# Kernel optimization log

Measured on AMD Instinct MI355X. Metric: run time of the kernel, lower is better.

Reference implementation:

```python
import jax, jax.numpy as jnp
import numpy as np


def _gcn_layer(x, W, b, row, col, num_nodes):
    # x: [N, F_in]; W: [F_in, F_out]; row/col: [E2] (with self-loops appended)
    xw = x @ W  # [N, F_out]
    ones = jnp.ones(row.shape[0], dtype=xw.dtype)
    deg = jax.ops.segment_sum(ones, col, num_segments=num_nodes)  # in-degree incl. self-loop
    dinv = jnp.where(deg > 0, jax.lax.rsqrt(deg), 0.0)
    norm = dinv[row] * dinv[col]  # [E2]
    msg = xw[row] * norm[:, None]  # gather + per-edge scale
    out = jax.ops.segment_sum(msg, col, num_segments=num_nodes)  # scatter-add to targets
    return out + b


def setup_inputs() -> dict:
    key = jax.random.key(0)
    k1, k2, k3, k4, k5 = jax.random.split(key, 5)
    N, E, F_in, F_hid = 100000, 640000, 128, 128
    x = jax.random.normal(k1, (N, F_in), dtype=jnp.float32)
    edge_index = jax.random.randint(k2, (2, E), 0, N, dtype=jnp.int64)
    # Glorot-style init like PyG GCNConv
    s1 = (6.0 / (F_in + F_hid)) ** 0.5
    W1 = jax.random.uniform(k3, (F_in, F_hid), jnp.float32, -s1, s1)
    b1 = jnp.zeros((F_hid,), jnp.float32)
    s2 = (6.0 / (F_hid + F_hid)) ** 0.5
    W2 = jax.random.uniform(k4, (F_hid, F_hid), jnp.float32, -s2, s2)
    b2 = jnp.zeros((F_hid,), jnp.float32)
    return {"x": x, "edge_index": edge_index, "W1": W1, "b1": b1, "W2": W2, "b2": b2}


def reference(x, edge_index, W1, b1, W2, b2):
    N = x.shape[0]
    # GCN adds self-loops before symmetric normalization (add_self_loops=True default)
    self_idx = jnp.arange(N, dtype=edge_index.dtype)
    row = jnp.concatenate([edge_index[0], self_idx])
    col = jnp.concatenate([edge_index[1], self_idx])
    h = _gcn_layer(x, W1, b1, row, col, N)
    h = jax.nn.relu(h)
    # dropout is identity in eval mode (training=False)
    out = _gcn_layer(h, W2, b2, row, col, N)
    return out
```

## Files before the change

### kernel.cpp

```cpp
#include <hip/hip_runtime.h>
#include <cstdint>
#include <cstddef>


typedef unsigned int u32;
typedef unsigned short u16;
typedef __attribute__((ext_vector_type(8))) short short8;
typedef __attribute__((ext_vector_type(4))) float f32x4;

__device__ __forceinline__ float bf2f(u32 lo16) {
  union { u32 u; float f; } c; c.u = lo16 << 16; return c.f;
}
__device__ __forceinline__ u32 f2bf(float f) {
  union { float f; u32 u; } c; c.f = f;
  return (c.u + 0x7fffu + ((c.u >> 16) & 1u)) >> 16;
}

__global__ __launch_bounds__(256) void zero_i32_kernel(int* __restrict__ p, int n) {
  int i = blockIdx.x * 256 + threadIdx.x;
  if (i < n) p[i] = 0;
}

__global__ __launch_bounds__(256) void count_kernel(
    const int* __restrict__ cols, const int* __restrict__ rows,
    int* __restrict__ cnt, int E, int N) {
  int e = blockIdx.x * 256 + threadIdx.x;
  if (e >= E) return;
  int c = cols[e];
  int r = rows[e];
  if ((unsigned)c >= (unsigned)N || (unsigned)r >= (unsigned)N) return;
  atomicAdd(&cnt[c], 1);
}

__global__ __launch_bounds__(256) void dinv_kernel(
    const int* __restrict__ cnt, float* __restrict__ dinv, int N) {
  int i = blockIdx.x * 256 + threadIdx.x;
  if (i >= N) return;
  dinv[i] = rsqrtf((float)cnt[i] + 1.0f);
}

__global__ __launch_bounds__(256) void wt_kernel(
    const float* __restrict__ W, u16* __restrict__ Wt) {
  int idx = blockIdx.x * 256 + threadIdx.x;
  int k = idx >> 7, n = idx & 127;
  Wt[n * 128 + k] = (u16)f2bf(W[idx]);
}

__global__ __launch_bounds__(256) void scan1_kernel(
    const int* __restrict__ cnt, int* __restrict__ rowptr,
    int* __restrict__ bsum, int N) {
  __shared__ int sd[256];
  int t = threadIdx.x;
  int base = blockIdx.x * 1024 + t * 4;
  int c0 = (base + 0 < N) ? cnt[base + 0] : 0;
  int c1 = (base + 1 < N) ? cnt[base + 1] : 0;
  int c2 = (base + 2 < N) ? cnt[base + 2] : 0;
  int c3 = (base + 3 < N) ? cnt[base + 3] : 0;
  int s = c0 + c1 + c2 + c3;
  sd[t] = s;
  __syncthreads();
  for (int off = 1; off < 256; off <<= 1) {
    int v = (t >= off) ? sd[t - off] : 0;
    __syncthreads();
    sd[t] += v;
    __syncthreads();
  }
  int excl = sd[t] - s;
  if (base + 0 < N) rowptr[base + 0] = excl;
  if (base + 1 < N) rowptr[base + 1] = excl + c0;
  if (base + 2 < N) rowptr[base + 2] = excl + c0 + c1;
  if (base + 3 < N) rowptr[base + 3] = excl + c0 + c1 + c2;
  if (t == 255) bsum[blockIdx.x] = sd[255];
}

__global__ __launch_bounds__(128) void scan2_kernel(
    const int* __restrict__ bsum, int* __restrict__ bsum2,
    int* __restrict__ rowptr, int NB, int N) {
  __shared__ int sd[128];
  int t = threadIdx.x;
  int v = (t < NB) ? bsum[t] : 0;
  sd[t] = v;
  __syncthreads();
  for (int off = 1; off < 128; off <<= 1) {
    int u = (t >= off) ? sd[t - off] : 0;
    __syncthreads();
    sd[t] += u;
    __syncthreads();
  }
  bsum2[t] = sd[t] - v;
  if (t == NB - 1) rowptr[N] = sd[t];
}

__global__ __launch_bounds__(256) void scan3_kernel(
    int* __restrict__ rowptr, const int* __restrict__ bsum2, int N) {
  int t = threadIdx.x;
  int b = blockIdx.x;
  int base = b * 1024 + t * 4;
  int add = bsum2[b];
#pragma unroll
  for (int k = 0; k < 4; k++)
    if (base + k < N) rowptr[base + k] += add;
}

__global__ __launch_bounds__(256) void fill_kernel(
    const int* __restrict__ cols, const int* __restrict__ rows,
    const int* __restrict__ rowptr, int* __restrict__ cursor,
    int* __restrict__ adj, int E, int N) {
  int e = blockIdx.x * 256 + threadIdx.x;
  if (e >= E) return;
  int c = cols[e];
  int r = rows[e];
  if ((unsigned)c >= (unsigned)N || (unsigned)r >= (unsigned)N) return;
  int pos = atomicAdd(&cursor[c], 1);
  adj[rowptr[c] + pos] = r;
}

template <int A_BF16>
__global__ __launch_bounds__(256) void gemm_mfma_kernel(
    const void* __restrict__ Av, const u16* __restrict__ Wt,
    const float* __restrict__ dinv, u16* __restrict__ C, int M) {
  __shared__ u16 Ws[128][136];
  __shared__ float dv_s[128];
  const int tid = threadIdx.x;
  const int row0 = blockIdx.x * 128;

  {
    const uint4* src = (const uint4*)Wt;
#pragma unroll
    for (int i = 0; i < 8; i++) {
      int linear = tid + i * 256;
      int n = linear >> 4;
      int kq = linear & 15;
      *(uint4*)&Ws[n][kq * 8] = src[linear];
    }
  }
  if (tid < 128) {
    int gr = row0 + tid;
    dv_s[tid] = (gr < M) ? dinv[gr] : 0.f;
  }
  __syncthreads();

  const int wave = tid >> 6;
  const int lane = tid & 63;
  const int lm = lane & 15;
  const int quad = lane >> 4;
  const int m0 = wave * 32;

  f32x4 acc[2][8];
#pragma unroll
  for (int mt = 0; mt < 2; mt++)
#pragma unroll
    for (int nt = 0; nt < 8; nt++) acc[mt][nt] = (f32x4){0.f, 0.f, 0.f, 0.f};

#pragma unroll
  for (int k0 = 0; k0 < 128; k0 += 32) {
    short8 bfrag[8];
#pragma unroll
    for (int nt = 0; nt < 8; nt++)
      bfrag[nt] = *(const short8*)&Ws[nt * 16 + lm][k0 + quad * 8];

    short8 afrag[2];
#pragma unroll
    for (int mt = 0; mt < 2; mt++) {
      int gr = row0 + m0 + mt * 16 + lm;
      short8 f = (short8){0, 0, 0, 0, 0, 0, 0, 0};
      if (gr < M) {
        if (A_BF16) {
          f = *(const short8*)((const u16*)Av + (size_t)gr * 128 + k0 + quad * 8);
        } else {
          const float* Af = (const float*)Av + (size_t)gr * 128 + k0 + quad * 8;
          float4 v0 = *(const float4*)Af;
          float4 v1 = *(const float4*)(Af + 4);
          f[0] = (short)f2bf(v0.x); f[1] = (short)f2bf(v0.y);
          f[2] = (short)f2bf(v0.z); f[3] = (short)f2bf(v0.w);
          f[4] = (short)f2bf(v1.x); f[5] = (short)f2bf(v1.y);
          f[6] = (short)f2bf(v1.z); f[7] = (short)f2bf(v1.w);
        }
      }
      afrag[mt] = f;
    }

#pragma unroll
    for (int mt = 0; mt < 2; mt++)
#pragma unroll
      for (int nt = 0; nt < 8; nt++)
        acc[mt][nt] = __builtin_amdgcn_mfma_f32_16x16x32_bf16(
            afrag[mt], bfrag[nt], acc[mt][nt], 0, 0, 0);
  }

#pragma unroll
  for (int mt = 0; mt < 2; mt++) {
    int rbase = m0 + mt * 16 + quad * 4;
#pragma unroll
    for (int r = 0; r < 4; r++) {
      int lrow = rbase + r;
      int grow = row0 + lrow;
      if (grow < M) {
        float dv = dv_s[lrow];
        u16* Crow = C + (size_t)grow * 128 + lm;
#pragma unroll
        for (int nt = 0; nt < 8; nt++)
          Crow[nt * 16] = (u16)f2bf(acc[mt][nt][r] * dv);
      }
    }
  }
}

template <int RELU, int OUT_BF16>
__global__ __launch_bounds__(256) void aggregate_kernel(
    const u32* __restrict__ xws, const int* __restrict__ rowptr,
    const int* __restrict__ adj, const float* __restrict__ dinv,
    const float* __restrict__ bias, void* __restrict__ out, int N) {
  int node = blockIdx.x * 4 + (threadIdx.x >> 6);
  if (node >= N) return;
  int lane = threadIdx.x & 63;

  u32 sv = xws[(size_t)node * 64 + lane];
  float accx = bf2f(sv & 0xffff);
  float accy = bf2f(sv >> 16);

  int beg = rowptr[node];
  int end = rowptr[node + 1];
  int j = beg;
  for (; j + 4 <= end; j += 4) {
    int s0 = adj[j], s1 = adj[j + 1], s2 = adj[j + 2], s3 = adj[j + 3];
    float m0 = 1.f, m1 = 1.f, m2 = 1.f, m3 = 1.f;
    if ((unsigned)s0 >= (unsigned)N) { s0 = 0; m0 = 0.f; }
    if ((unsigned)s1 >= (unsigned)N) { s1 = 0; m1 = 0.f; }
    if ((unsigned)s2 >= (unsigned)N) { s2 = 0; m2 = 0.f; }
    if ((unsigned)s3 >= (unsigned)N) { s3 = 0; m3 = 0.f; }
    u32 v0 = xws[(size_t)s0 * 64 + lane];
    u32 v1 = xws[(size_t)s1 * 64 + lane];
    u32 v2 = xws[(size_t)s2 * 64 + lane];
    u32 v3 = xws[(size_t)s3 * 64 + lane];
    accx = fmaf(m0, bf2f(v0 & 0xffff), accx); accy = fmaf(m0, bf2f(v0 >> 16), accy);
    accx = fmaf(m1, bf2f(v1 & 0xffff), accx); accy = fmaf(m1, bf2f(v1 >> 16), accy);
    accx = fmaf(m2, bf2f(v2 & 0xffff), accx); accy = fmaf(m2, bf2f(v2 >> 16), accy);
    accx = fmaf(m3, bf2f(v3 & 0xffff), accx); accy = fmaf(m3, bf2f(v3 >> 16), accy);
  }
  for (; j < end; j++) {
    int s = adj[j];
    float m = 1.f;
    if ((unsigned)s >= (unsigned)N) { s = 0; m = 0.f; }
    u32 v = xws[(size_t)s * 64 + lane];
    accx = fmaf(m, bf2f(v & 0xffff), accx);
    accy = fmaf(m, bf2f(v >> 16), accy);
  }

  float di = dinv[node];
  float2 bv = ((const float2*)bias)[lane];
  float ox = fmaf(di, accx, bv.x);
  float oy = fmaf(di, accy, bv.y);
  if (RELU) { ox = fmaxf(ox, 0.f); oy = fmaxf(oy, 0.f); }
  if (OUT_BF16) {
    ((u32*)out)[(size_t)node * 64 + lane] = f2bf(ox) | (f2bf(oy) << 16);
  } else {
    ((float2*)out)[(size_t)node * 64 + lane] = make_float2(ox, oy);
  }
}

extern "C" void kernel_launch(void* const* d_in, const int* in_sizes, int n_in,
                              void* d_out, int out_size, void* d_ws, size_t ws_size,
                              hipStream_t stream) {
  const float* x  = (const float*)d_in[0];
  const int*   ei = (const int*)d_in[1];
  const float* W1 = (const float*)d_in[2];
  const float* b1 = (const float*)d_in[3];
  const float* W2 = (const float*)d_in[4];
  const float* b2 = (const float*)d_in[5];
  float* out = (float*)d_out;

  const int F = 128;
  const int N = in_sizes[0] / F;
  const int E = in_sizes[1] / 2;
  const int* rows = ei;
  const int* cols = ei + E;

  u16*   bufXW  = (u16*)d_ws;
  u16*   bufH   = bufXW + (size_t)N * F;
  float* dinv   = (float*)(bufH + (size_t)N * F);
  int*   cnt    = (int*)(dinv + N);
  int*   rowptr = cnt + N;
  int*   adj    = rowptr + (N + 1);
  int*   bsum   = adj + E;
  int*   bsum2  = bsum + 128;
  u16*   Wt1    = (u16*)(bsum2 + 128);
  u16*   Wt2    = Wt1 + 128 * 128;

  const int NB = (N + 1023) / 1024;
  int eblocks = (E + 255) / 256;
  int nblocks = (N + 255) / 256;

  zero_i32_kernel<<<nblocks, 256, 0, stream>>>(cnt, N);
  count_kernel<<<eblocks, 256, 0, stream>>>(cols, rows, cnt, E, N);
  dinv_kernel<<<nblocks, 256, 0, stream>>>(cnt, dinv, N);
  scan1_kernel<<<NB, 256, 0, stream>>>(cnt, rowptr, bsum, N);
  scan2_kernel<<<1, 128, 0, stream>>>(bsum, bsum2, rowptr, NB, N);
  scan3_kernel<<<NB, 256, 0, stream>>>(rowptr, bsum2, N);
  zero_i32_kernel<<<nblocks, 256, 0, stream>>>(cnt, N);
  fill_kernel<<<eblocks, 256, 0, stream>>>(cols, rows, rowptr, cnt, adj, E, N);
  wt_kernel<<<64, 256, 0, stream>>>(W1, Wt1);
  wt_kernel<<<64, 256, 0, stream>>>(W2, Wt2);

  int gblocks = (N + 127) / 128;
  int ablocks = (N + 3) / 4;
  gemm_mfma_kernel<0><<<gblocks, 256, 0, stream>>>(x, Wt1, dinv, bufXW, N);
  aggregate_kernel<1, 1><<<ablocks, 256, 0, stream>>>(
      (const u32*)bufXW, rowptr, adj, dinv, b1, bufH, N);
  gemm_mfma_kernel<1><<<gblocks, 256, 0, stream>>>(bufH, Wt2, dinv, bufXW, N);
  aggregate_kernel<0, 0><<<ablocks, 256, 0, stream>>>(
      (const u32*)bufXW, rowptr, adj, dinv, b2, out, N);
}
```

Baseline: 292.5 us.

## Fuse setup kernels, stage GEMM output via LDS, widen aggregate gather per lane

Folds the dinv computation into scan1, merges the two weight-transpose launches into one, and reuses the count array as a decrementing cursor in fill so the second zeroing pass goes away. The GEMM epilogue now stages bf16 results in shared memory and writes them as coalesced 16-byte stores instead of scattered 2-byte stores. The aggregation kernel uses 32 lanes per node, each loading 8 bytes, and gathers 8 neighbours per iteration to raise memory-level parallelism. In exchange the edge order within each adjacency list is reversed, which can change floating-point summation order.

```diff
diff --git a/kernel.cpp b/kernel.cpp
--- a/kernel.cpp
+++ b/kernel.cpp
@@ -32,23 +32,20 @@
   atomicAdd(&cnt[c], 1);
 }
 
-__global__ __launch_bounds__(256) void dinv_kernel(
-    const int* __restrict__ cnt, float* __restrict__ dinv, int N) {
-  int i = blockIdx.x * 256 + threadIdx.x;
-  if (i >= N) return;
-  dinv[i] = rsqrtf((float)cnt[i] + 1.0f);
-}
-
 __global__ __launch_bounds__(256) void wt_kernel(
-    const float* __restrict__ W, u16* __restrict__ Wt) {
-  int idx = blockIdx.x * 256 + threadIdx.x;
+    const float* __restrict__ W1, const float* __restrict__ W2,
+    u16* __restrict__ Wt1, u16* __restrict__ Wt2) {
+  int b = blockIdx.x;
+  const float* W = (b < 64) ? W1 : W2;
+  u16* Wt = (b < 64) ? Wt1 : Wt2;
+  int idx = (b & 63) * 256 + threadIdx.x;
   int k = idx >> 7, n = idx & 127;
   Wt[n * 128 + k] = (u16)f2bf(W[idx]);
 }
 
 __global__ __launch_bounds__(256) void scan1_kernel(
     const int* __restrict__ cnt, int* __restrict__ rowptr,
-    int* __restrict__ bsum, int N) {
+    int* __restrict__ bsum, float* __restrict__ dinv, int N) {
   __shared__ int sd[256];
   int t = threadIdx.x;
   int base = blockIdx.x * 1024 + t * 4;
@@ -56,6 +53,10 @@
   int c1 = (base + 1 < N) ? cnt[base + 1] : 0;
   int c2 = (base + 2 < N) ? cnt[base + 2] : 0;
   int c3 = (base + 3 < N) ? cnt[base + 3] : 0;
+  if (base + 0 < N) dinv[base + 0] = rsqrtf((float)c0 + 1.0f);
+  if (base + 1 < N) dinv[base + 1] = rsqrtf((float)c1 + 1.0f);
+  if (base + 2 < N) dinv[base + 2] = rsqrtf((float)c2 + 1.0f);
+  if (base + 3 < N) dinv[base + 3] = rsqrtf((float)c3 + 1.0f);
   int s = c0 + c1 + c2 + c3;
   sd[t] = s;
   __syncthreads();
@@ -104,15 +105,15 @@
 
 __global__ __launch_bounds__(256) void fill_kernel(
     const int* __restrict__ cols, const int* __restrict__ rows,
-    const int* __restrict__ rowptr, int* __restrict__ cursor,
+    const int* __restrict__ rowptr, int* __restrict__ cnt,
     int* __restrict__ adj, int E, int N) {
   int e = blockIdx.x * 256 + threadIdx.x;
   if (e >= E) return;
   int c = cols[e];
   int r = rows[e];
   if ((unsigned)c >= (unsigned)N || (unsigned)r >= (unsigned)N) return;
-  int pos = atomicAdd(&cursor[c], 1);
-  adj[rowptr[c] + pos] = r;
+  int pos = atomicSub(&cnt[c], 1) - 1;
+  if (pos >= 0) adj[rowptr[c] + pos] = r;
 }
 
 template <int A_BF16>
@@ -188,74 +189,87 @@
             afrag[mt], bfrag[nt], acc[mt][nt], 0, 0, 0);
   }
 
+  __syncthreads();
 #pragma unroll
   for (int mt = 0; mt < 2; mt++) {
     int rbase = m0 + mt * 16 + quad * 4;
 #pragma unroll
     for (int r = 0; r < 4; r++) {
       int lrow = rbase + r;
-      int grow = row0 + lrow;
-      if (grow < M) {
-        float dv = dv_s[lrow];
-        u16* Crow = C + (size_t)grow * 128 + lm;
-#pragma unroll
-        for (int nt = 0; nt < 8; nt++)
-          Crow[nt * 16] = (u16)f2bf(acc[mt][nt][r] * dv);
-      }
-    }
+      float dv = dv_s[lrow];
+#pragma unroll
+      for (int nt = 0; nt < 8; nt++)
+        Ws[lrow][nt * 16 + lm] = (u16)f2bf(acc[mt][nt][r] * dv);
+    }
+  }
+  __syncthreads();
+#pragma unroll
+  for (int i = 0; i < 8; i++) {
+    int linear = tid + i * 256;
+    int row = linear >> 4;
+    int c8 = linear & 15;
+    int grow = row0 + row;
+    if (grow < M)
+      *(uint4*)(C + (size_t)grow * 128 + c8 * 8) = *(const uint4*)&Ws[row][c8 * 8];
   }
 }
 
 template <int RELU, int OUT_BF16>
 __global__ __launch_bounds__(256) void aggregate_kernel(
-    const u32* __restrict__ xws, const int* __restrict__ rowptr,
+    const uint2* __restrict__ xws, const int* __restrict__ rowptr,
     const int* __restrict__ adj, const float* __restrict__ dinv,
     const float* __restrict__ bias, void* __restrict__ out, int N) {
-  int node = blockIdx.x * 4 + (threadIdx.x >> 6);
+  int node = blockIdx.x * 8 + (threadIdx.x >> 5);
   if (node >= N) return;
-  int lane = threadIdx.x & 63;
-
-  u32 sv = xws[(size_t)node * 64 + lane];
-  float accx = bf2f(sv & 0xffff);
-  float accy = bf2f(sv >> 16);
+  int lane = threadIdx.x & 31;
+
+  uint2 sv = xws[(size_t)node * 32 + lane];
+  float a0 = bf2f(sv.x & 0xffff), a1 = bf2f(sv.x >> 16);
+  float a2 = bf2f(sv.y & 0xffff), a3 = bf2f(sv.y >> 16);
 
   int beg = rowptr[node];
   int end = rowptr[node + 1];
-  int j = beg;
-  for (; j + 4 <= end; j += 4) {
-    int s0 = adj[j], s1 = adj[j + 1], s2 = adj[j + 2], s3 = adj[j + 3];
-    float m0 = 1.f, m1 = 1.f, m2 = 1.f, m3 = 1.f;
-    if ((unsigned)s0 >= (unsigned)N) { s0 = 0; m0 = 0.f; }
-    if ((unsigned)s1 >= (unsigned)N) { s1 = 0; m1 = 0.f; }
-    if ((unsigned)s2 >= (unsigned)N) { s2 = 0; m2 = 0.f; }
-    if ((unsigned)s3 >= (unsigned)N) { s3 = 0; m3 = 0.f; }
-    u32 v0 = xws[(size_t)s0 * 64 + lane];
-    u32 v1 = xws[(size_t)s1 * 64 + lane];
-    u32 v2 = xws[(size_t)s2 * 64 + lane];
-    u32 v3 = xws[(size_t)s3 * 64 + lane];
-    accx = fmaf(m0, bf2f(v0 & 0xffff), accx); accy = fmaf(m0, bf2f(v0 >> 16), accy);
-    accx = fmaf(m1, bf2f(v1 & 0xffff), accx); accy = fmaf(m1, bf2f(v1 >> 16), accy);
-    accx = fmaf(m2, bf2f(v2 & 0xffff), accx); accy = fmaf(m2, bf2f(v2 >> 16), accy);
-    accx = fmaf(m3, bf2f(v3 & 0xffff), accx); accy = fmaf(m3, bf2f(v3 >> 16), accy);
-  }
-  for (; j < end; j++) {
-    int s = adj[j];
-    float m = 1.f;
-    if ((unsigned)s >= (unsigned)N) { s = 0; m = 0.f; }
-    u32 v = xws[(size_t)s * 64 + lane];
-    accx = fmaf(m, bf2f(v & 0xffff), accx);
-    accy = fmaf(m, bf2f(v >> 16), accy);
+  for (int j = beg; j < end; j += 8) {
+    int sidx[8];
+    float msk[8];
+#pragma unroll
+    for (int k = 0; k < 8; k++) {
+      int jj = j + k;
+      int s = (jj < end) ? adj[jj] : -1;
+      float m = 1.f;
+      if ((unsigned)s >= (unsigned)N) { s = 0; m = 0.f; }
+      sidx[k] = s;
+      msk[k] = m;
+    }
+    uint2 v[8];
+#pragma unroll
+    for (int k = 0; k < 8; k++) v[k] = xws[(size_t)sidx[k] * 32 + lane];
+#pragma unroll
+    for (int k = 0; k < 8; k++) {
+      a0 = fmaf(msk[k], bf2f(v[k].x & 0xffff), a0);
+      a1 = fmaf(msk[k], bf2f(v[k].x >> 16), a1);
+      a2 = fmaf(msk[k], bf2f(v[k].y & 0xffff), a2);
+      a3 = fmaf(msk[k], bf2f(v[k].y >> 16), a3);
+    }
   }
 
   float di = dinv[node];
-  float2 bv = ((const float2*)bias)[lane];
-  float ox = fmaf(di, accx, bv.x);
-  float oy = fmaf(di, accy, bv.y);
-  if (RELU) { ox = fmaxf(ox, 0.f); oy = fmaxf(oy, 0.f); }
+  float4 bv = ((const float4*)bias)[lane];
+  float o0 = fmaf(di, a0, bv.x);
+  float o1 = fmaf(di, a1, bv.y);
+  float o2 = fmaf(di, a2, bv.z);
+  float o3 = fmaf(di, a3, bv.w);
+  if (RELU) {
+    o0 = fmaxf(o0, 0.f); o1 = fmaxf(o1, 0.f);
+    o2 = fmaxf(o2, 0.f); o3 = fmaxf(o3, 0.f);
+  }
   if (OUT_BF16) {
-    ((u32*)out)[(size_t)node * 64 + lane] = f2bf(ox) | (f2bf(oy) << 16);
+    uint2 p;
+    p.x = f2bf(o0) | (f2bf(o1) << 16);
+    p.y = f2bf(o2) | (f2bf(o3) << 16);
+    ((uint2*)out)[(size_t)node * 32 + lane] = p;
   } else {
-    ((float2*)out)[(size_t)node * 64 + lane] = make_float2(ox, oy);
+    ((float4*)out)[(size_t)node * 32 + lane] = make_float4(o0, o1, o2, o3);
   }
 }
 
@@ -293,21 +307,18 @@
 
   zero_i32_kernel<<<nblocks, 256, 0, stream>>>(cnt, N);
   count_kernel<<<eblocks, 256, 0, stream>>>(cols, rows, cnt, E, N);
-  dinv_kernel<<<nblocks, 256, 0, stream>>>(cnt, dinv, N);
-  scan1_kernel<<<NB, 256, 0, stream>>>(cnt, rowptr, bsum, N);
+  wt_kernel<<<128, 256, 0, stream>>>(W1, W2, Wt1, Wt2);
+  scan1_kernel<<<NB, 256, 0, stream>>>(cnt, rowptr, bsum, dinv, N);
   scan2_kernel<<<1, 128, 0, stream>>>(bsum, bsum2, rowptr, NB, N);
   scan3_kernel<<<NB, 256, 0, stream>>>(rowptr, bsum2, N);
-  zero_i32_kernel<<<nblocks, 256, 0, stream>>>(cnt, N);
   fill_kernel<<<eblocks, 256, 0, stream>>>(cols, rows, rowptr, cnt, adj, E, N);
-  wt_kernel<<<64, 256, 0, stream>>>(W1, Wt1);
-  wt_kernel<<<64, 256, 0, stream>>>(W2, Wt2);
 
   int gblocks = (N + 127) / 128;
-  int ablocks = (N + 3) / 4;
+  int ablocks = (N + 7) / 8;
   gemm_mfma_kernel<0><<<gblocks, 256, 0, stream>>>(x, Wt1, dinv, bufXW, N);
   aggregate_kernel<1, 1><<<ablocks, 256, 0, stream>>>(
-      (const u32*)bufXW, rowptr, adj, dinv, b1, bufH, N);
+      (const uint2*)bufXW, rowptr, adj, dinv, b1, bufH, N);
   gemm_mfma_kernel<1><<<gblocks, 256, 0, stream>>>(bufH, Wt2, dinv, bufXW, N);
   aggregate_kernel<0, 0><<<ablocks, 256, 0, stream>>>(
-      (const u32*)bufXW, rowptr, adj, dinv, b2, out, N);
-}
+      (const uint2*)bufXW, rowptr, adj, dinv, b2, out, N);
+}
```

New measurement: 270.4 us. -7.6%, faster.
